# Kernel tuning notes

Hardware: AMD Instinct MI355X
Metric: run time of the kernel (lower is better)

Reference implementation:

```python
import jax, jax.numpy as jnp
import numpy as np

N, E, B = 50000, 800000, 512
DIN, H, A, BT = 128, 256, 40, 5


def _ln(h, g, b):
    m = jnp.mean(h, -1, keepdims=True)
    v = jnp.mean((h - m) ** 2, -1, keepdims=True)
    return (h - m) * jax.lax.rsqrt(v + 1e-5) * g + b


def _gcn(x, w, b, src, dst, n):
    # PyG GCNConv: add self-loops, symmetric D^-1/2 (A+I) D^-1/2 normalization
    h = x @ w
    loop = jnp.arange(n)
    s = jnp.concatenate([src, loop])
    d = jnp.concatenate([dst, loop])
    deg = jax.ops.segment_sum(jnp.ones(s.shape[0], h.dtype), d, num_segments=n)
    dinv = jax.lax.rsqrt(jnp.maximum(deg, 1.0))
    coef = (dinv[s] * dinv[d])[:, None]
    return jax.ops.segment_sum(coef * h[s], d, num_segments=n) + b


def _mlp2(x, w1, b1, w2, b2):
    return jax.nn.relu(x @ w1 + b1) @ w2 + b2


def _mlp3(x, w1, b1, w2, b2, w3, b3):
    h = jax.nn.relu(x @ w1 + b1)
    h = jax.nn.relu(h @ w2 + b2)
    return h @ w3 + b3


def setup_inputs() -> dict:
    key = jax.random.key(0)
    ks = iter(jax.random.split(key, 64))
    p = lambda shape: jax.random.normal(next(ks), shape, jnp.float32) * 0.05
    inp = {}
    inp["x"] = jax.random.normal(next(ks), (N, DIN), jnp.float32)
    inp["edge_index"] = jax.random.randint(next(ks), (2, E), 0, N)
    inp["batch"] = jnp.sort(jax.random.randint(next(ks), (N,), 0, B))
    inp["new_node_indices"] = jax.random.randint(next(ks), (B,), 0, N)
    inp["focus_node_indices"] = jax.random.randint(next(ks), (B,), 0, N)
    inp["num_graphs"] = B
    inp["conv_w0"] = p((DIN, H)); inp["conv_b0"] = p((H,))
    inp["conv_w1"] = p((H, H)); inp["conv_b1"] = p((H,))
    inp["conv_w2"] = p((H, H)); inp["conv_b2"] = p((H,))
    for i in range(3):
        inp[f"ln_g{i}"] = jnp.ones((H,), jnp.float32)
        inp[f"ln_b{i}"] = jnp.zeros((H,), jnp.float32)
    inp["res_w0"] = p((DIN, H)); inp["res_b0"] = p((H,))
    inp["stop_w1"] = p((H, H)); inp["stop_b1"] = p((H,))
    inp["stop_w2"] = p((H, 1)); inp["stop_b2"] = p((1,))
    inp["addn_w1"] = p((H, H)); inp["addn_b1"] = p((H,))
    inp["addn_w2"] = p((H, A)); inp["addn_b2"] = p((A,))
    inp["addb_w1"] = p((H, H)); inp["addb_b1"] = p((H,))
    inp["addb_w2"] = p((H, BT)); inp["addb_b2"] = p((BT,))
    inp["edge_w1"] = p((2 * H, H)); inp["edge_b1"] = p((H,))
    inp["edge_w2"] = p((H, H // 2)); inp["edge_b2"] = p((H // 2,))
    inp["edge_w3"] = p((H // 2, 1)); inp["edge_b3"] = p((1,))
    inp["bond_w1"] = p((2 * H, H)); inp["bond_b1"] = p((H,))
    inp["bond_w2"] = p((H, H // 2)); inp["bond_b2"] = p((H // 2,))
    inp["bond_w3"] = p((H // 2, BT)); inp["bond_b3"] = p((BT,))
    return inp


def reference(x, edge_index, batch, new_node_indices, focus_node_indices, num_graphs,
              conv_w0, conv_b0, conv_w1, conv_b1, conv_w2, conv_b2,
              ln_g0, ln_b0, ln_g1, ln_b1, ln_g2, ln_b2,
              res_w0, res_b0,
              stop_w1, stop_b1, stop_w2, stop_b2,
              addn_w1, addn_b1, addn_w2, addn_b2,
              addb_w1, addb_b1, addb_w2, addb_b2,
              edge_w1, edge_b1, edge_w2, edge_b2, edge_w3, edge_b3,
              bond_w1, bond_b1, bond_w2, bond_b2, bond_w3, bond_b3):
    n = x.shape[0]
    src, dst = edge_index[0], edge_index[1]
    conv_params = [(conv_w0, conv_b0), (conv_w1, conv_b1), (conv_w2, conv_b2)]
    ln_params = [(ln_g0, ln_b0), (ln_g1, ln_b1), (ln_g2, ln_b2)]
    h = x
    for i in range(3):
        h_in = h
        cw, cb = conv_params[i]
        lg, lb = ln_params[i]
        h = _gcn(h, cw, cb, src, dst, n)
        h = jax.nn.relu(_ln(h, lg, lb))  # dropout: eval mode (identity)
        res = h_in @ res_w0 + res_b0 if i == 0 else h_in
        h = h + res
    node_embeddings = h  # [N, H]
    # global mean pool over graphs
    counts = jax.ops.segment_sum(jnp.ones(n, h.dtype), batch, num_segments=num_graphs)
    graph_embedding = jax.ops.segment_sum(node_embeddings, batch, num_segments=num_graphs) / jnp.maximum(counts, 1.0)[:, None]
    stop_logits = _mlp2(graph_embedding, stop_w1, stop_b1, stop_w2, stop_b2)
    add_node_logits = _mlp2(graph_embedding, addn_w1, addn_b1, addn_w2, addn_b2)
    add_bond_logits = _mlp2(node_embeddings[focus_node_indices], addb_w1, addb_b1, addb_w2, addb_b2)
    # pair each node with its graph's newly added node
    new_node_embeddings = node_embeddings[new_node_indices]  # [B, H]
    pair = jnp.concatenate([node_embeddings, new_node_embeddings[batch]], axis=1)  # [N, 2H]
    edge_selection_logits = _mlp3(pair, edge_w1, edge_b1, edge_w2, edge_b2, edge_w3, edge_b3)
    bond_type_logits = _mlp3(pair, bond_w1, bond_b1, bond_w2, bond_b2, bond_w3, bond_b3)
    return (stop_logits, add_node_logits, add_bond_logits, node_embeddings,
            edge_selection_logits, bond_type_logits)
```

## Files before the change

### kernel.cpp

```cpp
#include <hip/hip_runtime.h>

typedef short bf16x8 __attribute__((ext_vector_type(8)));
typedef float f32x4 __attribute__((ext_vector_type(4)));
typedef unsigned short u16;
typedef u16 u16x8 __attribute__((ext_vector_type(8)));

__device__ __forceinline__ float bf2f(u16 u) {
  union { float f; unsigned int i; } x; x.i = ((unsigned int)u) << 16; return x.f;
}
__device__ __forceinline__ u16 f2bf(float f) {
  union { float f; unsigned int i; } x; x.f = f;
  unsigned int r = x.i + 0x7fffu + ((x.i >> 16) & 1u);
  return (u16)(r >> 16);
}
__device__ __forceinline__ void st_out_(void* out, size_t idx, float v, int f32) {
  if (f32) ((float*)out)[idx] = v;
  else ((u16*)out)[idx] = f2bf(v);
}

__global__ void k_detect(const u16* __restrict__ xx, int* flag) {
  int j = threadIdx.x;
  u16 u = xx[2 * j];
  int ex = (u >> 7) & 0xFF;
  int insane = (u != 0) && (ex < 100 || ex > 140);
  unsigned long long m = __ballot(insane);
  if (j == 0) flag[0] = (__popcll(m) > 8) ? 1 : 0;
}

__global__ void k_cvt_big(const void* __restrict__ src, u16* __restrict__ dst, int n,
                          const int* __restrict__ flag) {
  int i = blockIdx.x * 256 + threadIdx.x;
  if (i >= n) return;
  dst[i] = (*flag) ? f2bf(((const float*)src)[i]) : ((const u16*)src)[i];
}

#define NSEG 38
struct Cvt { const void* src[NSEG]; int off[NSEG + 1]; };
__global__ void k_cvt_all(Cvt c, u16* __restrict__ dst, int total, const int* __restrict__ flag) {
  int i = blockIdx.x * 256 + threadIdx.x;
  if (i >= total) return;
  int s = 0;
  #pragma unroll 1
  while (i >= c.off[s + 1]) s++;
  int j = i - c.off[s];
  dst[i] = (*flag) ? f2bf(((const float*)c.src[s])[j]) : ((const u16*)c.src[s])[j];
}

__global__ void k_padbias(const u16* __restrict__ rb, u16* cbz) {
  int i = blockIdx.x * 256 + threadIdx.x;
  if (i < 512) cbz[i] = (i < 256) ? (u16)0 : rb[i - 256];
}

struct Tr { const u16* src[8]; u16* dst[8]; int lk[8]; int nc[8]; int off[9]; };
__global__ void k_tr_all(Tr c, int total) {
  int i = blockIdx.x * 256 + threadIdx.x;
  if (i >= total) return;
  int s = 0;
  #pragma unroll 1
  while (i >= c.off[s + 1]) s++;
  int j = i - c.off[s];
  int K = 1 << c.lk[s];
  int nrow = j >> c.lk[s], k = j & (K - 1);
  c.dst[s][j] = c.src[s][k * c.nc[s] + nrow];
}

__global__ void k_init(int* deg, int* cursor, int n) {
  int i = blockIdx.x * 256 + threadIdx.x;
  if (i < n) { deg[i] = 1; cursor[i] = 0; }
}
__global__ void k_deg(const int* __restrict__ dst, int* deg, int e) {
  int i = blockIdx.x * 256 + threadIdx.x;
  if (i < e) atomicAdd(&deg[dst[i]], 1);
}
__global__ void k_dinv(const int* __restrict__ deg, float* dinv, int n) {
  int i = blockIdx.x * 256 + threadIdx.x;
  if (i < n) dinv[i] = rsqrtf((float)deg[i]);
}
#define SCB 4096
__global__ __launch_bounds__(256) void k_scanA(const int* __restrict__ deg, int* bsum, int n) {
  int b = blockIdx.x, t = threadIdx.x;
  int base = b * SCB;
  int s = 0;
  for (int j = t; j < SCB; j += 256) { int i = base + j; s += (i < n) ? deg[i] - 1 : 0; }
  int l = t & 63, wid = t >> 6;
  #pragma unroll
  for (int o = 32; o; o >>= 1) s += __shfl_xor(s, o);
  __shared__ int red[4];
  if (l == 0) red[wid] = s;
  __syncthreads();
  if (t == 0) bsum[b] = red[0] + red[1] + red[2] + red[3];
}
__global__ void k_scanB(int* bsum, int nb, int* off, int n) {
  if (threadIdx.x == 0) {
    int c = 0;
    for (int i = 0; i < nb; i++) { int v = bsum[i]; bsum[i] = c; c += v; }
    off[n] = c;
  }
}
__global__ __launch_bounds__(256) void k_scanC(const int* __restrict__ deg, const int* __restrict__ bsum,
                                               int* off, int n) {
  int b = blockIdx.x, t = threadIdx.x;
  int base = b * SCB + t * 16;
  int loc[16]; int s = 0;
  #pragma unroll
  for (int j = 0; j < 16; j++) { int i = base + j; loc[j] = s; s += (i < n) ? deg[i] - 1 : 0; }
  int l = t & 63, wid = t >> 6;
  int incl = s;
  #pragma unroll
  for (int o = 1; o < 64; o <<= 1) { int y = __shfl_up(incl, o); if (l >= o) incl += y; }
  int excl = incl - s;
  __shared__ int ws[4];
  if (l == 63) ws[wid] = incl;
  __syncthreads();
  int woff = 0;
  for (int w = 0; w < wid; w++) woff += ws[w];
  int pre = bsum[b] + woff + excl;
  #pragma unroll
  for (int j = 0; j < 16; j++) { int i = base + j; if (i < n) off[i] = pre + loc[j]; }
}
__global__ void k_csr(const int* __restrict__ src, const int* __restrict__ dst,
                      const int* __restrict__ off, int* cursor, int* csr_src, int e) {
  int i = blockIdx.x * 256 + threadIdx.x;
  if (i >= e) return;
  int d = dst[i], s = src[i];
  int slot = atomicAdd(&cursor[d], 1);
  csr_src[off[d] + slot] = s;
}

template <int EPI, int K>
__global__ __launch_bounds__(256) void gemm_p(
    const u16* __restrict__ A, int lda,
    const u16* __restrict__ Bt,
    u16* __restrict__ C, int ldc,
    int M, int NC,
    const u16* __restrict__ colbias,
    const float* __restrict__ rowbias, int rbld, const int* __restrict__ rowmap) {
  __shared__ u16 Bs[64 * K];
  __shared__ u16 As[4 * 2 * 1024];
  const int t = threadIdx.x;
  const int n0 = blockIdx.x * 64;
  const int m0 = blockIdx.y * 256;
  {
    const int ng = K >> 3;
    const int tot = 64 * ng;
    for (int i = t; i < tot; i += 256) {
      int c = i / ng, g = i - c * ng;
      u16x8 v = *reinterpret_cast<const u16x8*>(Bt + (size_t)(n0 + c) * K + g * 8);
      *reinterpret_cast<u16x8*>(&Bs[c * K + (g ^ (c & 7)) * 8]) = v;
    }
  }
  __syncthreads();

  const int wid = t >> 6, l = t & 63;
  const int rbase = m0 + wid * 64;
  const int lr = l & 15, lg = l >> 4;
  u16* Aw = &As[wid * 2048];
  const int jrow = l >> 3;
  const int gsw = (l & 7) ^ (l >> 3);

  auto stage = [&](int buf, int s) {
    int mi = s & 3, kh = s >> 2;
    u16* dst = Aw + buf * 1024;
    #pragma unroll
    for (int j = 0; j < 2; j++) {
      int row = rbase + mi * 16 + j * 8 + jrow;
      if (row >= M) row = M - 1;
      __builtin_amdgcn_global_load_lds(
          (const __attribute__((address_space(1))) unsigned int*)(A + (size_t)row * lda + kh * 64 + gsw * 8),
          (__attribute__((address_space(3))) unsigned int*)(dst + j * 512), 16, 0, 0);
    }
  };

  f32x4 acc[4][4] = {};
  bf16x8 bfr[2][4];
  const int S = (K >> 6) * 4;
  stage(0, 0);
  #pragma unroll
  for (int s = 0; s < S; s++) {
    const int buf = s & 1, mi = s & 3, kh = s >> 2;
    if (s + 1 < S) {
      stage(buf ^ 1, s + 1);
      asm volatile("s_waitcnt vmcnt(2)" ::: "memory");
    } else {
      asm volatile("s_waitcnt vmcnt(0)" ::: "memory");
    }
    __builtin_amdgcn_sched_barrier(0);
    if (mi == 0) {
      #pragma unroll
      for (int ks = 0; ks < 2; ks++)
        #pragma unroll
        for (int ni = 0; ni < 4; ni++) {
          int g = kh * 8 + ks * 4 + lg;
          bfr[ks][ni] = *reinterpret_cast<const bf16x8*>(&Bs[(ni * 16 + lr) * K + (g ^ (lr & 7)) * 8]);
        }
    }
    const u16* Ab = Aw + buf * 1024;
    #pragma unroll
    for (int ks = 0; ks < 2; ks++) {
      bf16x8 af = *reinterpret_cast<const bf16x8*>(&Ab[lr * 64 + ((ks * 4 + lg) ^ (lr & 7)) * 8]);
      #pragma unroll
      for (int ni = 0; ni < 4; ni++)
        acc[mi][ni] = __builtin_amdgcn_mfma_f32_16x16x32_bf16(af, bfr[ks][ni], acc[mi][ni], 0, 0, 0);
    }
  }

  #pragma unroll
  for (int mi = 0; mi < 4; mi++) {
    int rowi[4];
    #pragma unroll
    for (int r = 0; r < 4; r++) rowi[r] = rbase + mi * 16 + lg * 4 + r;
    float rbv[4][4];
    if (EPI == 3) {
      int rmv[4];
      #pragma unroll
      for (int r = 0; r < 4; r++) {
        int rr = rowi[r]; if (rr >= M) rr = M - 1;
        rmv[r] = rowmap[rr];
      }
      #pragma unroll
      for (int ni = 0; ni < 4; ni++)
        #pragma unroll
        for (int r = 0; r < 4; r++)
          rbv[ni][r] = rowbias[(size_t)rmv[r] * rbld + n0 + ni * 16 + lr];
    }
    #pragma unroll
    for (int ni = 0; ni < 4; ni++) {
      int col = n0 + ni * 16 + lr;
      float cbv = 0.f;
      if (EPI == 1 || EPI == 2) cbv = bf2f(colbias[col]);
      #pragma unroll
      for (int r = 0; r < 4; r++) {
        if (rowi[r] < M) {
          float v = acc[mi][ni][r];
          if (EPI == 1 || EPI == 2) v += cbv;
          if (EPI == 3) v += rbv[ni][r];
          if (EPI == 2 || EPI == 3) v = fmaxf(v, 0.f);
          C[(size_t)rowi[r] * ldc + col] = f2bf(v);
        }
      }
    }
  }
}

__global__ __launch_bounds__(256, 6) void k_agg(
    const u16* __restrict__ hw, int hwld, const u16* __restrict__ cb,
    const u16* __restrict__ lng, const u16* __restrict__ lnb,
    const u16* __restrict__ res, int resld, const float* __restrict__ dinv,
    const int* __restrict__ off, const int* __restrict__ csr_src,
    u16* __restrict__ hout, int n) {
  int l = threadIdx.x & 63;
  int v = blockIdx.x * 4 + (threadIdx.x >> 6);
  if (v >= n) return;
  const int half = l >> 5;
  const int c0 = (l & 31) * 8;
  float a[8] = {0, 0, 0, 0, 0, 0, 0, 0};
  int s = off[v], e = off[v + 1];
  int i = s;
  for (; i + 7 < e; i += 8) {
    int u0 = csr_src[i + half],     u1 = csr_src[i + 2 + half];
    int u2 = csr_src[i + 4 + half], u3 = csr_src[i + 6 + half];
    float w0 = dinv[u0], w1 = dinv[u1], w2 = dinv[u2], w3 = dinv[u3];
    u16x8 r0 = *reinterpret_cast<const u16x8*>(hw + (size_t)u0 * hwld + c0);
    u16x8 r1 = *reinterpret_cast<const u16x8*>(hw + (size_t)u1 * hwld + c0);
    u16x8 r2 = *reinterpret_cast<const u16x8*>(hw + (size_t)u2 * hwld + c0);
    u16x8 r3 = *reinterpret_cast<const u16x8*>(hw + (size_t)u3 * hwld + c0);
    #pragma unroll
    for (int j = 0; j < 8; j++)
      a[j] += w0 * bf2f(r0[j]) + w1 * bf2f(r1[j]) + w2 * bf2f(r2[j]) + w3 * bf2f(r3[j]);
  }
  for (; i < e; i += 2) {
    int idx = i + half;
    if (idx < e) {
      int u = csr_src[idx];
      float w = dinv[u];
      u16x8 r = *reinterpret_cast<const u16x8*>(hw + (size_t)u * hwld + c0);
      #pragma unroll
      for (int j = 0; j < 8; j++) a[j] += w * bf2f(r[j]);
    }
  }
  #pragma unroll
  for (int j = 0; j < 8; j++) a[j] += __shfl_xor(a[j], 32);
  float dv = dinv[v];
  u16x8 sv = *reinterpret_cast<const u16x8*>(hw + (size_t)v * hwld + c0);
  u16x8 cbv = *reinterpret_cast<const u16x8*>(cb + c0);
  float sum = 0.f;
  #pragma unroll
  for (int j = 0; j < 8; j++) {
    a[j] = dv * (dv * bf2f(sv[j]) + a[j]) + bf2f(cbv[j]);
    sum += a[j];
  }
  #pragma unroll
  for (int o = 16; o; o >>= 1) sum += __shfl_xor(sum, o);
  float mean = sum * (1.f / 256.f);
  float vs = 0.f;
  #pragma unroll
  for (int j = 0; j < 8; j++) { float d = a[j] - mean; vs += d * d; }
  #pragma unroll
  for (int o = 16; o; o >>= 1) vs += __shfl_xor(vs, o);
  float rs = rsqrtf(vs * (1.f / 256.f) + 1e-5f);
  u16x8 gv = *reinterpret_cast<const u16x8*>(lng + c0);
  u16x8 bv = *reinterpret_cast<const u16x8*>(lnb + c0);
  u16x8 rv = *reinterpret_cast<const u16x8*>(res + (size_t)v * resld + c0);
  u16x8 ov;
  #pragma unroll
  for (int j = 0; j < 8; j++)
    ov[j] = f2bf(fmaxf((a[j] - mean) * rs * bf2f(gv[j]) + bf2f(bv[j]), 0.f) + bf2f(rv[j]));
  if (half == 0)
    *reinterpret_cast<u16x8*>(hout + (size_t)v * 256 + c0) = ov;
}

__global__ __launch_bounds__(256) void k_pool(const u16* __restrict__ h, const int* __restrict__ batch,
                                              int n, float* gemb) {
  int g = blockIdx.x, c = threadIdx.x;
  int lo = 0, hi = n;
  while (lo < hi) { int mid = (lo + hi) >> 1; if (batch[mid] < g) lo = mid + 1; else hi = mid; }
  int s = lo;
  lo = s; hi = n;
  while (lo < hi) { int mid = (lo + hi) >> 1; if (batch[mid] < g + 1) lo = mid + 1; else hi = mid; }
  int e = lo;
  float acc = 0.f;
  for (int i = s; i < e; i++) acc += bf2f(h[(size_t)i * 256 + c]);
  int cnt = e - s; if (cnt < 1) cnt = 1;
  gemb[g * 256 + c] = acc / (float)cnt;
}

__global__ __launch_bounds__(256) void k_glin(const u16* __restrict__ h, const int* __restrict__ nidx,
                                              const u16* __restrict__ W, const u16* __restrict__ b1,
                                              float* g1, int ld, int ofs) {
  int b = blockIdx.x, t = threadIdx.x;
  __shared__ float sin_[256];
  sin_[t] = bf2f(h[(size_t)nidx[b] * 256 + t]);
  __syncthreads();
  float acc = bf2f(b1[t]);
  #pragma unroll 8
  for (int k = 0; k < 256; k++) acc += sin_[k] * bf2f(W[k * 256 + t]);
  g1[(size_t)b * ld + ofs + t] = acc;
}

template <int OUTD>
__global__ __launch_bounds__(256) void k_mlp2(const float* __restrict__ inf32,
                                              const u16* __restrict__ inbf, const int* __restrict__ idx,
                                              const u16* __restrict__ W1, const u16* __restrict__ b1,
                                              const u16* __restrict__ W2, const u16* __restrict__ b2,
                                              void* __restrict__ out, size_t obase,
                                              const int* __restrict__ flag) {
  int b = blockIdx.x, t = threadIdx.x;
  __shared__ float sin_[256];
  __shared__ float sh[256];
  sin_[t] = inf32 ? inf32[b * 256 + t] : bf2f(inbf[(size_t)idx[b] * 256 + t]);
  __syncthreads();
  float acc = bf2f(b1[t]);
  #pragma unroll 8
  for (int k = 0; k < 256; k++) acc += sin_[k] * bf2f(W1[k * 256 + t]);
  sh[t] = fmaxf(acc, 0.f);
  __syncthreads();
  if (t < OUTD) {
    float a2 = bf2f(b2[t]);
    #pragma unroll 8
    for (int k = 0; k < 256; k++) a2 += sh[k] * bf2f(W2[k * OUTD + t]);
    st_out_(out, obase + (size_t)b * OUTD + t, a2, *flag);
  }
}

__global__ __launch_bounds__(256) void k_final(const u16* __restrict__ t2e, const u16* __restrict__ t2b,
                                               const u16* __restrict__ w3e, const u16* __restrict__ b3e,
                                               const u16* __restrict__ w3b, const u16* __restrict__ b3b,
                                               void* __restrict__ out, size_t oe, size_t ob, int M,
                                               const int* __restrict__ flag) {
  int r = blockIdx.x * 4 + (threadIdx.x >> 6);
  int l = threadIdx.x & 63;
  if (r >= M) return;
  float p[6] = {0, 0, 0, 0, 0, 0};
  #pragma unroll
  for (int j = 0; j < 2; j++) {
    int k = l * 2 + j;
    float te = bf2f(t2e[(size_t)r * 128 + k]);
    float tb = bf2f(t2b[(size_t)r * 128 + k]);
    p[0] += te * bf2f(w3e[k]);
    #pragma unroll
    for (int q = 0; q < 5; q++) p[1 + q] += tb * bf2f(w3b[k * 5 + q]);
  }
  #pragma unroll
  for (int q = 0; q < 6; q++)
    #pragma unroll
    for (int o = 32; o; o >>= 1) p[q] += __shfl_xor(p[q], o);
  if (l == 0) {
    int f32 = *flag;
    st_out_(out, oe + r, p[0] + bf2f(b3e[0]), f32);
    #pragma unroll
    for (int q = 0; q < 5; q++)
      st_out_(out, ob + (size_t)r * 5 + q, p[1 + q] + bf2f(b3b[q]), f32);
  }
}

__global__ void k_emit8(const u16* __restrict__ src, void* __restrict__ out, size_t obase, int n8,
                        const int* __restrict__ flag) {
  int i = blockIdx.x * 256 + threadIdx.x;
  if (i >= n8) return;
  u16x8 v = reinterpret_cast<const u16x8*>(src)[i];
  if (*flag) {
    float4* fo = (float4*)((float*)out + obase);
    float4 lo, hi;
    lo.x = bf2f(v[0]); lo.y = bf2f(v[1]); lo.z = bf2f(v[2]); lo.w = bf2f(v[3]);
    hi.x = bf2f(v[4]); hi.y = bf2f(v[5]); hi.z = bf2f(v[6]); hi.w = bf2f(v[7]);
    fo[(size_t)i * 2] = lo; fo[(size_t)i * 2 + 1] = hi;
  } else {
    reinterpret_cast<u16x8*>((u16*)out + obase)[i] = v;
  }
}

extern "C" void kernel_launch(void* const* d_in, const int* in_sizes, int n_in,
                              void* d_out, int out_size, void* d_ws, size_t ws_size,
                              hipStream_t stream) {
  const int N = in_sizes[0] / 128;
  const int E = in_sizes[1] / 2;
  const int B = in_sizes[3];

  const int* ei    = (const int*)d_in[1];
  const int* srcp  = ei;
  const int* dstp  = ei + E;
  const int* batch = (const int*)d_in[2];
  const int* newi  = (const int*)d_in[3];
  const int* focus = (const int*)d_in[4];

  const size_t o_stop = 0;
  const size_t o_addn = (size_t)B;
  const size_t o_addb = (size_t)B + (size_t)B * 40;
  const size_t o_emb  = o_addb + (size_t)B * 5;
  const size_t o_esel = o_emb + (size_t)N * 256;
  const size_t o_bond = o_esel + (size_t)N;

  char* p = (char*)d_ws;
  auto alloc = [&](size_t bytes) -> void* {
    void* r = (void*)p;
    p += (bytes + 255) & ~(size_t)255;
    return r;
  };
  int* flag = (int*)alloc(4);
  static const int seg_din[NSEG] = {6,7,8,9,10,11, 12,13,14,15,16,17, 18,19,
                                    20,21,22,23, 24,25,26,27, 28,29,30,31,
                                    32,33,34,35,36,37, 38,39,40,41,42,43};
  static const int seg_len[NSEG] = {32768,256,65536,256,65536,256, 256,256,256,256,256,256,
                                    32768,256, 65536,256,256,1, 65536,256,10240,40,
                                    65536,256,1280,5, 131072,256,32768,128,128,1,
                                    131072,256,32768,128,640,5};
  int wtotal = 0;
  int seg_off[NSEG + 1];
  for (int i = 0; i < NSEG; i++) { seg_off[i] = wtotal; wtotal += seg_len[i]; }
  seg_off[NSEG] = wtotal;
  u16* wbf = (u16*)alloc((size_t)wtotal * 2);
  u16* wt_f0  = (u16*)alloc(512 * 128 * 2);
  u16* wt_cw1 = (u16*)alloc(256 * 256 * 2);
  u16* wt_cw2 = (u16*)alloc(256 * 256 * 2);
  u16* wt_t1  = (u16*)alloc(512 * 256 * 2);
  u16* wt_e2  = (u16*)alloc(128 * 256 * 2);
  u16* wt_b2  = (u16*)alloc(128 * 256 * 2);
  u16* cbz    = (u16*)alloc(512 * 2);
  int*   deg     = (int*)alloc((size_t)N * 4);
  int*   cursor  = (int*)alloc((size_t)N * 4);
  int*   off     = (int*)alloc((size_t)(N + 1) * 4);
  float* dinv    = (float*)alloc((size_t)N * 4);
  int*   bsum    = (int*)alloc(64 * 4);
  float* gemb    = (float*)alloc((size_t)B * 256 * 4);
  float* g1full  = (float*)alloc((size_t)B * 512 * 4);
  int*   csr_src = (int*)alloc((size_t)E * 4);
  u16*   xbf     = (u16*)alloc((size_t)N * 128 * 2);
  u16*   P1      = (u16*)alloc((size_t)N * 256 * 2);
  u16*   P2      = (u16*)alloc((size_t)N * 256 * 2);
  u16*   P3      = (u16*)alloc((size_t)N * 256 * 2);

  auto wseg = [&](int i) -> u16* { return wbf + seg_off[i]; };
  u16 *cw0 = wseg(0), *cb0 = wseg(1), *cw1 = wseg(2), *cb1 = wseg(3), *cw2 = wseg(4), *cb2 = wseg(5);
  u16 *lg0 = wseg(6), *lb0 = wseg(7), *lg1 = wseg(8), *lb1 = wseg(9), *lg2 = wseg(10), *lb2 = wseg(11);
  u16 *rw0 = wseg(12), *rb0 = wseg(13);
  u16 *sw1 = wseg(14), *sb1 = wseg(15), *sw2 = wseg(16), *sb2 = wseg(17);
  u16 *aw1 = wseg(18), *ab1 = wseg(19), *aw2 = wseg(20), *ab2 = wseg(21);
  u16 *bw1 = wseg(22), *bb1 = wseg(23), *bw2 = wseg(24), *bb2 = wseg(25);
  u16 *ew1 = wseg(26), *eb1 = wseg(27), *ew2 = wseg(28), *eb2 = wseg(29), *ew3 = wseg(30), *eb3 = wseg(31);
  u16 *qw1 = wseg(32), *qb1 = wseg(33), *qw2 = wseg(34), *qb2 = wseg(35), *qw3 = wseg(36), *qb3 = wseg(37);

  k_detect<<<1, 64, 0, stream>>>((const u16*)d_in[0], flag);
  k_cvt_big<<<(N * 128 + 255) / 256, 256, 0, stream>>>(d_in[0], xbf, N * 128, flag);
  Cvt cd;
  for (int i = 0; i < NSEG; i++) cd.src[i] = d_in[seg_din[i]];
  for (int i = 0; i <= NSEG; i++) cd.off[i] = seg_off[i];
  k_cvt_all<<<(wtotal + 255) / 256, 256, 0, stream>>>(cd, wbf, wtotal, flag);
  k_padbias<<<2, 256, 0, stream>>>(rb0, cbz);

  const int NB = (N + 255) / 256;
  const int EBk = (E + 255) / 256;
  const int NBS = (N + SCB - 1) / SCB;

  k_init<<<NB, 256, 0, stream>>>(deg, cursor, N);
  k_deg<<<EBk, 256, 0, stream>>>(dstp, deg, E);
  k_dinv<<<NB, 256, 0, stream>>>(deg, dinv, N);
  k_scanA<<<NBS, 256, 0, stream>>>(deg, bsum, N);
  k_scanB<<<1, 64, 0, stream>>>(bsum, NBS, off, N);
  k_scanC<<<NBS, 256, 0, stream>>>(deg, bsum, off, N);
  k_csr<<<EBk, 256, 0, stream>>>(srcp, dstp, off, cursor, csr_src, E);

  {
    Tr td;
    const u16* ts[8] = {cw0, rw0, cw1, cw2, ew1, qw1, ew2, qw2};
    u16* tdst[8] = {wt_f0, wt_f0 + 256 * 128, wt_cw1, wt_cw2, wt_t1, wt_t1 + 256 * 256, wt_e2, wt_b2};
    int tlk[8] = {7, 7, 8, 8, 8, 8, 8, 8};
    int tnc[8] = {256, 256, 256, 256, 256, 256, 128, 128};
    int tlen[8] = {32768, 32768, 65536, 65536, 65536, 65536, 32768, 32768};
    int tot = 0;
    for (int i = 0; i < 8; i++) {
      td.src[i] = ts[i]; td.dst[i] = tdst[i]; td.lk[i] = tlk[i]; td.nc[i] = tnc[i];
      td.off[i] = tot; tot += tlen[i];
    }
    td.off[8] = tot;
    k_tr_all<<<(tot + 255) / 256, 256, 0, stream>>>(td, tot);
  }

  const int MB = (N + 255) / 256;
  const int AGB = (N + 3) / 4;
  u16* PF = P1;

  gemm_p<1, 128><<<dim3(8, MB), 256, 0, stream>>>(xbf, 128, wt_f0, PF, 512, N, 512, cbz, nullptr, 0, nullptr);
  k_agg<<<AGB, 256, 0, stream>>>(PF, 512, cb0, lg0, lb0, PF + 256, 512, dinv, off, csr_src, P3, N);
  gemm_p<0, 256><<<dim3(4, MB), 256, 0, stream>>>(P3, 256, wt_cw1, P1, 256, N, 256, nullptr, nullptr, 0, nullptr);
  k_agg<<<AGB, 256, 0, stream>>>(P1, 256, cb1, lg1, lb1, P3, 256, dinv, off, csr_src, P2, N);
  gemm_p<0, 256><<<dim3(4, MB), 256, 0, stream>>>(P2, 256, wt_cw2, P1, 256, N, 256, nullptr, nullptr, 0, nullptr);
  k_agg<<<AGB, 256, 0, stream>>>(P1, 256, cb2, lg2, lb2, P2, 256, dinv, off, csr_src, P3, N);

  k_emit8<<<(N * 256 / 8 + 255) / 256, 256, 0, stream>>>(P3, d_out, o_emb, N * 256 / 8, flag);

  k_pool<<<B, 256, 0, stream>>>(P3, batch, N, gemb);
  k_glin<<<B, 256, 0, stream>>>(P3, newi, ew1 + 256 * 256, eb1, g1full, 512, 0);
  k_glin<<<B, 256, 0, stream>>>(P3, newi, qw1 + 256 * 256, qb1, g1full, 512, 256);
  k_mlp2<1><<<B, 256, 0, stream>>>(gemb, nullptr, nullptr, sw1, sb1, sw2, sb2, d_out, o_stop, flag);
  k_mlp2<40><<<B, 256, 0, stream>>>(gemb, nullptr, nullptr, aw1, ab1, aw2, ab2, d_out, o_addn, flag);
  k_mlp2<5><<<B, 256, 0, stream>>>(nullptr, P3, focus, bw1, bb1, bw2, bb2, d_out, o_addb, flag);

  u16* T1 = PF;
  gemm_p<3, 256><<<dim3(8, MB), 256, 0, stream>>>(P3, 256, wt_t1, T1, 512, N, 512, nullptr, g1full, 512, batch);
  u16* t2e = P3;
  u16* t2b = P3 + (size_t)N * 128;
  gemm_p<2, 256><<<dim3(2, MB), 256, 0, stream>>>(T1, 512, wt_e2, t2e, 128, N, 128, eb2, nullptr, 0, nullptr);
  gemm_p<2, 256><<<dim3(2, MB), 256, 0, stream>>>(T1 + 256, 512, wt_b2, t2b, 128, N, 128, qb2, nullptr, 0, nullptr);
  k_final<<<(N + 3) / 4, 256, 0, stream>>>(t2e, t2b, ew3, eb3, qw3, qb3, d_out, o_esel, o_bond, N, flag);
}
```

Measured before the change: 646.3 us.

## Deepen GEMM A-tile prefetch, widen aggregation gather, split pool accumulators

The GEMM A-staging moves from a two-buffer pipeline of 64-wide K chunks to a four-slot ring of 32-wide K chunks with two stages in flight, and the vmcnt waits are adjusted to match. The GCN aggregation kernel gains a 16-edge unrolled loop that issues eight independent row gathers before accumulating, which raises memory-level parallelism on the irregular loads. The pooling kernel uses four independent accumulators to break the serial add dependency. These are three separate latency-hiding tweaks in different kernels; the smaller K chunks mean more stages and more waits per GEMM, and the wider unroll raises register pressure in k_agg.

```diff
diff --git a/kernel.cpp b/kernel.cpp
--- a/kernel.cpp
+++ b/kernel.cpp
@@ -136,7 +136,7 @@
     const u16* __restrict__ colbias,
     const float* __restrict__ rowbias, int rbld, const int* __restrict__ rowmap) {
   __shared__ u16 Bs[64 * K];
-  __shared__ u16 As[4 * 2 * 1024];
+  __shared__ u16 As[4 * 4 * 512];
   const int t = threadIdx.x;
   const int n0 = blockIdx.x * 64;
   const int m0 = blockIdx.y * 256;
@@ -155,53 +155,43 @@
   const int rbase = m0 + wid * 64;
   const int lr = l & 15, lg = l >> 4;
   u16* Aw = &As[wid * 2048];
-  const int jrow = l >> 3;
-  const int gsw = (l & 7) ^ (l >> 3);
-
-  auto stage = [&](int buf, int s) {
-    int mi = s & 3, kh = s >> 2;
-    u16* dst = Aw + buf * 1024;
-    #pragma unroll
-    for (int j = 0; j < 2; j++) {
-      int row = rbase + mi * 16 + j * 8 + jrow;
-      if (row >= M) row = M - 1;
-      __builtin_amdgcn_global_load_lds(
-          (const __attribute__((address_space(1))) unsigned int*)(A + (size_t)row * lda + kh * 64 + gsw * 8),
-          (__attribute__((address_space(3))) unsigned int*)(dst + j * 512), 16, 0, 0);
-    }
+  const int srow = l >> 2;
+  const int sg = (l & 3) ^ (srow & 3);
+
+  auto stage = [&](int s) {
+    int mi = s & 3, kk = s >> 2;
+    int row = rbase + mi * 16 + srow;
+    if (row >= M) row = M - 1;
+    __builtin_amdgcn_global_load_lds(
+        (const __attribute__((address_space(1))) unsigned int*)(A + (size_t)row * lda + kk * 32 + sg * 8),
+        (__attribute__((address_space(3))) unsigned int*)(Aw + (s & 3) * 512), 16, 0, 0);
   };
 
   f32x4 acc[4][4] = {};
-  bf16x8 bfr[2][4];
-  const int S = (K >> 6) * 4;
-  stage(0, 0);
+  bf16x8 bfr[4];
+  const int S = K >> 3;
+  stage(0); stage(1);
   #pragma unroll
   for (int s = 0; s < S; s++) {
-    const int buf = s & 1, mi = s & 3, kh = s >> 2;
-    if (s + 1 < S) {
-      stage(buf ^ 1, s + 1);
-      asm volatile("s_waitcnt vmcnt(2)" ::: "memory");
-    } else {
-      asm volatile("s_waitcnt vmcnt(0)" ::: "memory");
-    }
+    const int buf = s & 3, mi = s & 3, kk = s >> 2;
+    if (s + 2 < S) stage(s + 2);
+    const int rem = (s + 2 < S) ? 2 : (S - 1 - s);
+    if (rem >= 2)      asm volatile("s_waitcnt vmcnt(2)" ::: "memory");
+    else if (rem == 1) asm volatile("s_waitcnt vmcnt(1)" ::: "memory");
+    else               asm volatile("s_waitcnt vmcnt(0)" ::: "memory");
     __builtin_amdgcn_sched_barrier(0);
     if (mi == 0) {
       #pragma unroll
-      for (int ks = 0; ks < 2; ks++)
-        #pragma unroll
-        for (int ni = 0; ni < 4; ni++) {
-          int g = kh * 8 + ks * 4 + lg;
-          bfr[ks][ni] = *reinterpret_cast<const bf16x8*>(&Bs[(ni * 16 + lr) * K + (g ^ (lr & 7)) * 8]);
-        }
-    }
-    const u16* Ab = Aw + buf * 1024;
-    #pragma unroll
-    for (int ks = 0; ks < 2; ks++) {
-      bf16x8 af = *reinterpret_cast<const bf16x8*>(&Ab[lr * 64 + ((ks * 4 + lg) ^ (lr & 7)) * 8]);
-      #pragma unroll
-      for (int ni = 0; ni < 4; ni++)
-        acc[mi][ni] = __builtin_amdgcn_mfma_f32_16x16x32_bf16(af, bfr[ks][ni], acc[mi][ni], 0, 0, 0);
-    }
+      for (int ni = 0; ni < 4; ni++) {
+        int g = kk * 4 + lg;
+        bfr[ni] = *reinterpret_cast<const bf16x8*>(&Bs[(ni * 16 + lr) * K + (g ^ (lr & 7)) * 8]);
+      }
+    }
+    const u16* Ab = Aw + buf * 512;
+    bf16x8 af = *reinterpret_cast<const bf16x8*>(&Ab[lr * 32 + (lg ^ (lr & 3)) * 8]);
+    #pragma unroll
+    for (int ni = 0; ni < 4; ni++)
+      acc[mi][ni] = __builtin_amdgcn_mfma_f32_16x16x32_bf16(af, bfr[ni], acc[mi][ni], 0, 0, 0);
   }
 
   #pragma unroll
@@ -256,6 +246,24 @@
   float a[8] = {0, 0, 0, 0, 0, 0, 0, 0};
   int s = off[v], e = off[v + 1];
   int i = s;
+  for (; i + 15 < e; i += 16) {
+    int uu[8];
+    #pragma unroll
+    for (int q = 0; q < 8; q++) uu[q] = csr_src[i + 2 * q + half];
+    float ww[8];
+    #pragma unroll
+    for (int q = 0; q < 8; q++) ww[q] = dinv[uu[q]];
+    u16x8 rr[8];
+    #pragma unroll
+    for (int q = 0; q < 8; q++) rr[q] = *reinterpret_cast<const u16x8*>(hw + (size_t)uu[q] * hwld + c0);
+    #pragma unroll
+    for (int j = 0; j < 8; j++) {
+      float t0 = 0.f;
+      #pragma unroll
+      for (int q = 0; q < 8; q++) t0 += ww[q] * bf2f(rr[q][j]);
+      a[j] += t0;
+    }
+  }
   for (; i + 7 < e; i += 8) {
     int u0 = csr_src[i + half],     u1 = csr_src[i + 2 + half];
     int u2 = csr_src[i + 4 + half], u3 = csr_src[i + 6 + half];
@@ -318,8 +326,16 @@
   lo = s; hi = n;
   while (lo < hi) { int mid = (lo + hi) >> 1; if (batch[mid] < g + 1) lo = mid + 1; else hi = mid; }
   int e = lo;
-  float acc = 0.f;
-  for (int i = s; i < e; i++) acc += bf2f(h[(size_t)i * 256 + c]);
+  float a0 = 0.f, a1 = 0.f, a2 = 0.f, a3 = 0.f;
+  int i = s;
+  for (; i + 3 < e; i += 4) {
+    a0 += bf2f(h[(size_t)i * 256 + c]);
+    a1 += bf2f(h[(size_t)(i + 1) * 256 + c]);
+    a2 += bf2f(h[(size_t)(i + 2) * 256 + c]);
+    a3 += bf2f(h[(size_t)(i + 3) * 256 + c]);
+  }
+  for (; i < e; i++) a0 += bf2f(h[(size_t)i * 256 + c]);
+  float acc = (a0 + a1) + (a2 + a3);
   int cnt = e - s; if (cnt < 1) cnt = 1;
   gemb[g * 256 + c] = acc / (float)cnt;
 }
```

Result: slower. 752.2 us (+16.4%).
